# Kernel tuning notes

Hardware: AMD Instinct MI355X
Metric: run time of the kernel (lower is better)

Reference implementation:

```python
import jax, jax.numpy as jnp
import numpy as np

B, C_IN, C_OUT, C_KEY, N = 8, 512, 512, 256, 2048


def setup_inputs() -> dict:
    key = jax.random.key(0)
    k1, k2, k3, k4 = jax.random.split(key, 4)
    x = jax.random.normal(k1, (B, C_IN, N), dtype=jnp.float32)
    # Conv1d(kernel=1, bias=False) weights -> plain linear maps over channel dim
    Wq = jax.random.normal(k2, (C_KEY, C_IN), dtype=jnp.float32) * (1.0 / np.sqrt(C_IN))
    Wk = jax.random.normal(k3, (C_KEY, C_IN), dtype=jnp.float32) * (1.0 / np.sqrt(C_IN))
    Wv = jax.random.normal(k4, (C_OUT, C_IN), dtype=jnp.float32) * (1.0 / np.sqrt(C_IN))
    return {"x": x, "Wq": Wq, "Wk": Wk, "Wv": Wv}


def reference(x, Wq, Wk, Wv):
    # 1x1 conv projections: [B, C, N] -> [B, Ck/Co, N]
    q = jnp.einsum("oc,bcn->bon", Wq, x)
    k = jnp.einsum("oc,bcn->bon", Wk, x)
    v = jnpqv = jnp.einsum("oc,bcn->bon", Wv, x)
    # sim_map[b,i,j] = sum_c k[b,c,i] * q[b,c,j]  (unscaled)
    sim = jnp.einsum("bci,bcj->bij", k, q)  # [B, N, N]
    attn = jax.nn.softmax(sim, axis=-1)
    # out = value @ sim_map, then permute(0,2,1) -> [B, N, C_out]
    out = jnp.einsum("bck,bkm->bmc", jnpqv, attn)
    return out
```

## Files before the change

### kernel.cpp

```cpp
#include <hip/hip_runtime.h>

typedef _Float16 half8 __attribute__((ext_vector_type(8)));
typedef _Float16 half4v __attribute__((ext_vector_type(4)));
typedef _Float16 half2v __attribute__((ext_vector_type(2)));
typedef float f32x4 __attribute__((ext_vector_type(4)));

#define ASYNC_CP16(gp, lp)                                       \
  __builtin_amdgcn_global_load_lds(                              \
      (const __attribute__((address_space(1))) void*)(gp),       \
      (__attribute__((address_space(3))) void*)(lp), 16, 0, 0)

static __device__ __forceinline__ half8 mulw(half8 a, half8 s) {
  half8 o;
#pragma unroll
  for (int j = 0; j < 8; j++) o[j] = a[j] * s[j];
  return o;
}

__global__ __launch_bounds__(256) void conv_w(const float* __restrict__ Wq,
                                              const float* __restrict__ Wk,
                                              const float* __restrict__ Wv,
                                              _Float16* __restrict__ Wb) {
  int idx = blockIdx.x * 256 + threadIdx.x;
  int row = idx >> 9;
  float v;
  if (row < 256)      v = Wq[idx];
  else if (row < 512) v = Wk[idx - 256 * 512];
  else                v = Wv[idx - 512 * 512];
  Wb[idx] = (_Float16)v;
}

__global__ __launch_bounds__(256) void conv_xT(const float* __restrict__ x,
                                               _Float16* __restrict__ xT) {
  __shared__ float T[32][33];
  const int b = blockIdx.z;
  const int n0 = blockIdx.x * 32, c0 = blockIdx.y * 32;
  const int t = threadIdx.x;
  const float* xb = x + (size_t)b * 512 * 2048;
  const int n2 = t & 15, cr = t >> 4;
#pragma unroll
  for (int r = 0; r < 2; r++) {
    int c = cr + r * 16;
    float2 v = *(const float2*)&xb[(size_t)(c0 + c) * 2048 + n0 + n2 * 2];
    T[c][n2 * 2] = v.x;
    T[c][n2 * 2 + 1] = v.y;
  }
  __syncthreads();
  _Float16* xtb = xT + (size_t)b * 2048 * 512;
  const int c2 = t & 15, nr = t >> 4;
#pragma unroll
  for (int r = 0; r < 2; r++) {
    int n = nr + r * 16;
    half2v h;
    h[0] = (_Float16)T[c2 * 2][n];
    h[1] = (_Float16)T[c2 * 2 + 1][n];
    *(half2v*)&xtb[(size_t)(n0 + n) * 512 + c0 + c2 * 2] = h;
  }
}

template <typename OutT, int BUFS, int MODE>
__global__ __launch_bounds__(256) void gemm_nt(
    const _Float16* __restrict__ A, const _Float16* __restrict__ B,
    OutT* __restrict__ C, OutT* __restrict__ C2, int K, int lda, int ldb,
    int ldc, int ldc2, long sA, long sB, long sC, float* __restrict__ pm,
    float* __restrict__ ps) {
  A += (size_t)blockIdx.z * sA;
  B += (size_t)blockIdx.z * sB;
  C += (size_t)blockIdx.z * sC;
  if constexpr (MODE == 1) C2 += (size_t)blockIdx.z * sC;
  const int m_blk = blockIdx.y * 128, n_blk = blockIdx.x * 128;

  __shared__ _Float16 As[BUFS][4096];
  __shared__ _Float16 Bs[BUFS][4096];

  const int t = threadIdx.x;
  const int lane = t & 63, wave = t >> 6;
  const int quad = lane >> 4, l16 = lane & 15;
  const int wm = (wave & 1) * 64, wn = (wave >> 1) * 64;

  const int srow = 16 * wave + (lane >> 2);
  const int schunk = (lane & 3) ^ ((lane >> 3) & 3);
  const _Float16* gA0 = A + (size_t)(m_blk + srow) * lda + schunk * 8;
  const _Float16* gA1 = gA0 + (size_t)64 * lda;
  const _Float16* gB0 = B + (size_t)(n_blk + srow) * ldb + schunk * 8;
  const _Float16* gB1 = gB0 + (size_t)64 * ldb;
  const int lofs = wave * 512 + lane * 8;

  const int rchunk = (quad ^ ((l16 >> 1) & 3)) * 8;

  f32x4 acc[4][4] = {};

#pragma unroll
  for (int pb = 0; pb < BUFS - 1; pb++) {
    if (pb * 32 < K) {
      ASYNC_CP16(gA0 + pb * 32, &As[pb][lofs]);
      ASYNC_CP16(gA1 + pb * 32, &As[pb][lofs + 2048]);
      ASYNC_CP16(gB0 + pb * 32, &Bs[pb][lofs]);
      ASYNC_CP16(gB1 + pb * 32, &Bs[pb][lofs + 2048]);
    }
  }

  int ib = 0;
  for (int k0 = 0; k0 < K; k0 += 32) {
    if constexpr (BUFS == 3) {
      if (k0 + 32 < K)
        asm volatile("s_waitcnt vmcnt(4)\n\ts_barrier" ::: "memory");
      else
        asm volatile("s_waitcnt vmcnt(0)\n\ts_barrier" ::: "memory");
    } else {
      asm volatile("s_waitcnt vmcnt(0)\n\ts_barrier" ::: "memory");
    }
    if (k0 + (BUFS - 1) * 32 < K) {
      int nb = ib + BUFS - 1;
      if (nb >= BUFS) nb -= BUFS;
      const int ko = k0 + (BUFS - 1) * 32;
      ASYNC_CP16(gA0 + ko, &As[nb][lofs]);
      ASYNC_CP16(gA1 + ko, &As[nb][lofs + 2048]);
      ASYNC_CP16(gB0 + ko, &Bs[nb][lofs]);
      ASYNC_CP16(gB1 + ko, &Bs[nb][lofs + 2048]);
    }
    half8 af[4], bf[4];
#pragma unroll
    for (int i = 0; i < 4; i++) {
      af[i] = *(const half8*)&As[ib][(wm + i * 16 + l16) * 32 + rchunk];
      bf[i] = *(const half8*)&Bs[ib][(wn + i * 16 + l16) * 32 + rchunk];
    }
#pragma unroll
    for (int i = 0; i < 4; i++)
#pragma unroll
      for (int j = 0; j < 4; j++)
        acc[i][j] =
            __builtin_amdgcn_mfma_f32_16x16x32_f16(af[i], bf[j], acc[i][j], 0, 0, 0);
    ib++;
    if (ib == BUFS) ib = 0;
  }

  if constexpr (MODE == 2) {
#pragma unroll
    for (int j = 0; j < 4; j++) {
      const int n0 = n_blk + wn + j * 16 + l16;
      float mx = acc[0][j][0];
#pragma unroll
      for (int i = 0; i < 4; i++)
#pragma unroll
        for (int r = 0; r < 4; r++) mx = fmaxf(mx, acc[i][j][r]);
      mx = fmaxf(mx, __shfl_xor(mx, 16, 64));
      mx = fmaxf(mx, __shfl_xor(mx, 32, 64));
      float es = 0.f;
#pragma unroll
      for (int i = 0; i < 4; i++) {
        const int m0 = m_blk + wm + i * 16 + quad * 4;
#pragma unroll
        for (int r = 0; r < 4; r++) {
          _Float16 h = (_Float16)__expf(acc[i][j][r] - mx);
          C[(size_t)(m0 + r) * ldc + n0] = h;
          es += (float)h;
        }
      }
      es += __shfl_xor(es, 16, 64);
      es += __shfl_xor(es, 32, 64);
      if (quad == 0) {
        size_t o =
            ((size_t)blockIdx.z * 32 + blockIdx.y * 2 + (wave & 1)) * 2048 + n0;
        pm[o] = mx;
        ps[o] = es;
      }
    }
  } else {
#pragma unroll
    for (int i = 0; i < 4; i++) {
      const int m0 = m_blk + wm + i * 16 + quad * 4;
#pragma unroll
      for (int j = 0; j < 4; j++) {
        const int n0 = n_blk + wn + j * 16 + l16;
        if constexpr (MODE == 1) {
          if (m_blk < 512) {
            half4v h;
#pragma unroll
            for (int r = 0; r < 4; r++) h[r] = (_Float16)acc[i][j][r];
            *(half4v*)&C[(size_t)n0 * ldc + m0] = h;
          } else {
#pragma unroll
            for (int r = 0; r < 4; r++)
              C2[(size_t)(m0 - 512 + r) * ldc2 + n0] = (OutT)acc[i][j][r];
          }
        } else {
#pragma unroll
          for (int r = 0; r < 4; r++)
            C[(size_t)(m0 + r) * ldc + n0] = (OutT)acc[i][j][r];
        }
      }
    }
  }
}

__global__ __launch_bounds__(256) void colstats2(const float* __restrict__ pm,
                                                 const float* __restrict__ ps,
                                                 _Float16* __restrict__ scl) {
  const int idx = blockIdx.x * 256 + threadIdx.x;
  const int b = idx >> 11, col = idx & 2047;
  const float* pmb = pm + (size_t)b * 32 * 2048 + col;
  const float* psb = ps + (size_t)b * 32 * 2048 + col;
  float pv[32];
  float m = -3.0e38f;
#pragma unroll
  for (int i = 0; i < 32; i++) {
    pv[i] = pmb[(size_t)i * 2048];
    m = fmaxf(m, pv[i]);
  }
  float s = 0.f;
#pragma unroll
  for (int i = 0; i < 32; i++) {
    pv[i] = __expf(pv[i] - m);
    s += psb[(size_t)i * 2048] * pv[i];
  }
  const float inv = 1.0f / s;
  _Float16* so = scl + (size_t)b * 32 * 2048 + col;
#pragma unroll
  for (int i = 0; i < 32; i++) so[(size_t)i * 2048] = (_Float16)(pv[i] * inv);
}

__global__ __launch_bounds__(256) void gemm_av(const _Float16* __restrict__ P,
                                               const _Float16* __restrict__ V,
                                               const _Float16* __restrict__ scl,
                                               float* __restrict__ C,
                                               int cbatch) {
  int lin = blockIdx.x, z, idx;
  if (cbatch == 8) {
    z = lin & 7;
    idx = lin >> 3;
  } else {
    z = lin >> 6;
    idx = lin & 63;
  }
  const int n_blk = (idx & 3) * 128;
  const int m_blk = (idx >> 2) * 128;
  P += (size_t)z * 2048 * 2048;
  V += (size_t)z * 512 * 2048;
  scl += ((size_t)z * 32 + (m_blk >> 6)) * 2048;
  C += (size_t)z * 2048 * 512;

  __shared__ _Float16 As[2][4096];
  __shared__ _Float16 Bs[3][4096];

  const int t = threadIdx.x;
  const int lane = t & 63, wave = t >> 6;
  const int quad = lane >> 4, l16 = lane & 15;
  const int wm = (wave & 1) * 64, wn = (wave >> 1) * 64;

  const int srow = 16 * wave + (lane >> 2);
  const int schunk = (lane & 3) ^ ((lane >> 3) & 3);
  const _Float16* gA0 = P + (size_t)(m_blk + srow) * 2048 + schunk * 8;
  const _Float16* gA1 = gA0 + (size_t)64 * 2048;
  const _Float16* gB0 = V + (size_t)(n_blk + srow) * 2048 + schunk * 8;
  const _Float16* gB1 = gB0 + (size_t)64 * 2048;
  const _Float16* gS0 = scl + schunk * 8;
  const _Float16* gS1 = gS0 + 2048;
  const int lofs = wave * 512 + lane * 8;
  const int rchunk = (quad ^ ((l16 >> 1) & 3)) * 8;

  f32x4 acc[4][4] = {};

  ASYNC_CP16(gB0, &Bs[0][lofs]);
  ASYNC_CP16(gB1, &Bs[0][lofs + 2048]);
  ASYNC_CP16(gB0 + 32, &Bs[1][lofs]);
  ASYNC_CP16(gB1 + 32, &Bs[1][lofs + 2048]);
  {
    half8 a0 = *(const half8*)gA0;
    half8 a1 = *(const half8*)gA1;
    half8 s0 = *(const half8*)gS0;
    half8 s1 = *(const half8*)gS1;
    *(half8*)&As[0][lofs] = mulw(a0, s0);
    *(half8*)&As[0][lofs + 2048] = mulw(a1, s1);
  }
  half8 an0 = *(const half8*)(gA0 + 32);
  half8 an1 = *(const half8*)(gA1 + 32);
  half8 sn0 = *(const half8*)(gS0 + 32);
  half8 sn1 = *(const half8*)(gS1 + 32);
  __syncthreads();

  int ibA = 0, ibB = 0;
  for (int k0 = 0; k0 < 2048; k0 += 32) {
    const bool m1 = (k0 + 32 < 2048), m2 = (k0 + 64 < 2048);
    if (m2) {
      int nb = ibB + 2;
      if (nb >= 3) nb -= 3;
      ASYNC_CP16(gB0 + k0 + 64, &Bs[nb][lofs]);
      ASYNC_CP16(gB1 + k0 + 64, &Bs[nb][lofs + 2048]);
    }
    half8 a20, a21, s20, s21;
    if (m2) {
      a20 = *(const half8*)(gA0 + k0 + 64);
      a21 = *(const half8*)(gA1 + k0 + 64);
      s20 = *(const half8*)(gS0 + k0 + 64);
      s21 = *(const half8*)(gS1 + k0 + 64);
    }
    half8 af[4], bf[4];
#pragma unroll
    for (int i = 0; i < 4; i++) {
      af[i] = *(const half8*)&As[ibA][(wm + i * 16 + l16) * 32 + rchunk];
      bf[i] = *(const half8*)&Bs[ibB][(wn + i * 16 + l16) * 32 + rchunk];
    }
#pragma unroll
    for (int i = 0; i < 4; i++)
#pragma unroll
      for (int j = 0; j < 4; j++)
        acc[i][j] =
            __builtin_amdgcn_mfma_f32_16x16x32_f16(af[i], bf[j], acc[i][j], 0, 0, 0);
    if (m1) {
      *(half8*)&As[ibA ^ 1][lofs] = mulw(an0, sn0);
      *(half8*)&As[ibA ^ 1][lofs + 2048] = mulw(an1, sn1);
      if (m2) {
        an0 = a20;
        an1 = a21;
        sn0 = s20;
        sn1 = s21;
      }
      asm volatile("s_waitcnt vmcnt(6) lgkmcnt(0)\n\ts_barrier" ::: "memory");
    }
    ibA ^= 1;
    ibB++;
    if (ibB == 3) ibB = 0;
  }

#pragma unroll
  for (int i = 0; i < 4; i++) {
    const int m0 = m_blk + wm + i * 16 + quad * 4;
#pragma unroll
    for (int j = 0; j < 4; j++) {
      const int n0 = n_blk + wn + j * 16 + l16;
#pragma unroll
      for (int r = 0; r < 4; r++) C[(size_t)(m0 + r) * 512 + n0] = acc[i][j][r];
    }
  }
}

extern "C" void kernel_launch(void* const* d_in, const int* in_sizes, int n_in,
                              void* d_out, int out_size, void* d_ws,
                              size_t ws_size, hipStream_t stream) {
  const float* x = (const float*)d_in[0];
  const float* Wq = (const float*)d_in[1];
  const float* Wk = (const float*)d_in[2];
  const float* Wv = (const float*)d_in[3];
  float* out = (float*)d_out;

  char* p = (char*)d_ws;
  auto alloc = [&](size_t bytes) -> char* {
    char* r = p;
    p += (bytes + 255) & ~(size_t)255;
    return r;
  };
  const size_t NB = 8, N = 2048, CIN = 512, CO = 512;
  _Float16* Wb = (_Float16*)alloc(1024 * 512 * sizeof(_Float16));
  _Float16* xT = (_Float16*)alloc(NB * N * CIN * sizeof(_Float16));
  _Float16* qkT = (_Float16*)alloc(NB * N * 512 * sizeof(_Float16));
  _Float16* v = (_Float16*)alloc(NB * CO * N * sizeof(_Float16));
  size_t base_used = (size_t)(p - (char*)d_ws);

  const size_t per_b =
      (size_t)N * N * 2 + 2 * 32 * N * 4 + 32 * N * 2 + 8192;
  int cb = 8;
  while (cb > 1 && base_used + (size_t)cb * per_b > ws_size) cb >>= 1;
  _Float16* simH = (_Float16*)alloc((size_t)cb * N * N * 2);
  float* pm = (float*)alloc((size_t)cb * 32 * N * 4);
  float* ps = (float*)alloc((size_t)cb * 32 * N * 4);
  _Float16* scl = (_Float16*)alloc((size_t)cb * 32 * N * 2);

  conv_w<<<dim3(1024 * 512 / 256), 256, 0, stream>>>(Wq, Wk, Wv, Wb);
  conv_xT<<<dim3(64, 16, 8), 256, 0, stream>>>(x, xT);

  gemm_nt<_Float16, 3, 1><<<dim3(16, 8, 8), 256, 0, stream>>>(
      Wb, xT, qkT, v, 512, 512, 512, 512, 2048, 0, (long)(N * CIN),
      (long)(N * 512), nullptr, nullptr);

  for (int b0 = 0; b0 < 8; b0 += cb) {
    const _Float16* qT = qkT + (size_t)b0 * N * 512;
    const _Float16* kT = qkT + (size_t)b0 * N * 512 + 256;
    gemm_nt<_Float16, 2, 2><<<dim3(16, 16, cb), 256, 0, stream>>>(
        qT, kT, simH, nullptr, 256, 512, 512, 2048, 0, (long)(N * 512),
        (long)(N * 512), (long)(N * N), pm, ps);
    colstats2<<<dim3(cb * 8), 256, 0, stream>>>(pm, ps, scl);
    gemm_av<<<dim3(64 * cb), 256, 0, stream>>>(
        simH, v + (size_t)b0 * CO * N, scl, out + (size_t)b0 * N * CO, cb);
  }
}
```

Baseline: 212.4 us.

## Load P operand fragments directly from global into registers, dropping A LDS tile

The P·V GEMM kernel no longer stages the scaled P tile through shared memory. Each wave now loads its own MFMA A-fragments (four rows of 16) straight from global memory into registers, two steps ahead, and applies the per-row scale before the MFMAs. This removes the LDS writes, the LDS reads and part of the barrier traffic for A, and frees shared memory. The cost is duplicate global loads across the two waves that share the same rows, less coalesced fragment-shaped loads, and more registers held in flight.

```diff
diff --git a/kernel.cpp b/kernel.cpp
--- a/kernel.cpp
+++ b/kernel.cpp
@@ -240,7 +240,6 @@
   scl += ((size_t)z * 32 + (m_blk >> 6)) * 2048;
   C += (size_t)z * 2048 * 512;
 
-  __shared__ _Float16 As[2][4096];
   __shared__ _Float16 Bs[3][4096];
 
   const int t = threadIdx.x;
@@ -250,14 +249,13 @@
 
   const int srow = 16 * wave + (lane >> 2);
   const int schunk = (lane & 3) ^ ((lane >> 3) & 3);
-  const _Float16* gA0 = P + (size_t)(m_blk + srow) * 2048 + schunk * 8;
-  const _Float16* gA1 = gA0 + (size_t)64 * 2048;
   const _Float16* gB0 = V + (size_t)(n_blk + srow) * 2048 + schunk * 8;
   const _Float16* gB1 = gB0 + (size_t)64 * 2048;
-  const _Float16* gS0 = scl + schunk * 8;
-  const _Float16* gS1 = gS0 + 2048;
   const int lofs = wave * 512 + lane * 8;
   const int rchunk = (quad ^ ((l16 >> 1) & 3)) * 8;
+
+  const _Float16* gA = P + (size_t)(m_blk + wm + l16) * 2048 + quad * 8;
+  const _Float16* gS = scl + (wm >> 6) * 2048 + quad * 8;
 
   f32x4 acc[4][4] = {};
 
@@ -265,62 +263,60 @@
   ASYNC_CP16(gB1, &Bs[0][lofs + 2048]);
   ASYNC_CP16(gB0 + 32, &Bs[1][lofs]);
   ASYNC_CP16(gB1 + 32, &Bs[1][lofs + 2048]);
-  {
-    half8 a0 = *(const half8*)gA0;
-    half8 a1 = *(const half8*)gA1;
-    half8 s0 = *(const half8*)gS0;
-    half8 s1 = *(const half8*)gS1;
-    *(half8*)&As[0][lofs] = mulw(a0, s0);
-    *(half8*)&As[0][lofs + 2048] = mulw(a1, s1);
-  }
-  half8 an0 = *(const half8*)(gA0 + 32);
-  half8 an1 = *(const half8*)(gA1 + 32);
-  half8 sn0 = *(const half8*)(gS0 + 32);
-  half8 sn1 = *(const half8*)(gS1 + 32);
-  __syncthreads();
-
-  int ibA = 0, ibB = 0;
+  asm volatile("" ::: "memory");
+  half8 ac0 = *(const half8*)(gA);
+  half8 ac1 = *(const half8*)(gA + 16 * 2048);
+  half8 ac2 = *(const half8*)(gA + 32 * 2048);
+  half8 ac3 = *(const half8*)(gA + 48 * 2048);
+  half8 scc = *(const half8*)(gS);
+  half8 an0 = *(const half8*)(gA + 32);
+  half8 an1 = *(const half8*)(gA + 16 * 2048 + 32);
+  half8 an2 = *(const half8*)(gA + 32 * 2048 + 32);
+  half8 an3 = *(const half8*)(gA + 48 * 2048 + 32);
+  half8 scn = *(const half8*)(gS + 32);
+  asm volatile("s_waitcnt vmcnt(0)\n\ts_barrier" ::: "memory");
+
+  int ib = 0;
   for (int k0 = 0; k0 < 2048; k0 += 32) {
-    const bool m1 = (k0 + 32 < 2048), m2 = (k0 + 64 < 2048);
+    const bool m2 = (k0 + 64 < 2048);
+    half8 a20, a21, a22, a23, s2;
     if (m2) {
-      int nb = ibB + 2;
+      int nb = ib + 2;
       if (nb >= 3) nb -= 3;
       ASYNC_CP16(gB0 + k0 + 64, &Bs[nb][lofs]);
       ASYNC_CP16(gB1 + k0 + 64, &Bs[nb][lofs + 2048]);
-    }
-    half8 a20, a21, s20, s21;
-    if (m2) {
-      a20 = *(const half8*)(gA0 + k0 + 64);
-      a21 = *(const half8*)(gA1 + k0 + 64);
-      s20 = *(const half8*)(gS0 + k0 + 64);
-      s21 = *(const half8*)(gS1 + k0 + 64);
-    }
-    half8 af[4], bf[4];
-#pragma unroll
-    for (int i = 0; i < 4; i++) {
-      af[i] = *(const half8*)&As[ibA][(wm + i * 16 + l16) * 32 + rchunk];
-      bf[i] = *(const half8*)&Bs[ibB][(wn + i * 16 + l16) * 32 + rchunk];
-    }
+      asm volatile("" ::: "memory");
+      a20 = *(const half8*)(gA + k0 + 64);
+      a21 = *(const half8*)(gA + 16 * 2048 + k0 + 64);
+      a22 = *(const half8*)(gA + 32 * 2048 + k0 + 64);
+      a23 = *(const half8*)(gA + 48 * 2048 + k0 + 64);
+      s2 = *(const half8*)(gS + k0 + 64);
+    }
+    half8 bf[4];
+#pragma unroll
+    for (int j = 0; j < 4; j++)
+      bf[j] = *(const half8*)&Bs[ib][(wn + j * 16 + l16) * 32 + rchunk];
+    half8 am[4];
+    am[0] = mulw(ac0, scc);
+    am[1] = mulw(ac1, scc);
+    am[2] = mulw(ac2, scc);
+    am[3] = mulw(ac3, scc);
 #pragma unroll
     for (int i = 0; i < 4; i++)
 #pragma unroll
       for (int j = 0; j < 4; j++)
         acc[i][j] =
-            __builtin_amdgcn_mfma_f32_16x16x32_f16(af[i], bf[j], acc[i][j], 0, 0, 0);
-    if (m1) {
-      *(half8*)&As[ibA ^ 1][lofs] = mulw(an0, sn0);
-      *(half8*)&As[ibA ^ 1][lofs + 2048] = mulw(an1, sn1);
-      if (m2) {
-        an0 = a20;
-        an1 = a21;
-        sn0 = s20;
-        sn1 = s21;
-      }
-      asm volatile("s_waitcnt vmcnt(6) lgkmcnt(0)\n\ts_barrier" ::: "memory");
-    }
-    ibA ^= 1;
-    ibB++;
-    if (ibB == 3) ibB = 0;
+            __builtin_amdgcn_mfma_f32_16x16x32_f16(am[i], bf[j], acc[i][j], 0, 0, 0);
+    ac0 = an0; ac1 = an1; ac2 = an2; ac3 = an3; scc = scn;
+    if (m2) { an0 = a20; an1 = a21; an2 = a22; an3 = a23; scn = s2; }
+    if (k0 + 32 < 2048) {
+      if (m2)
+        asm volatile("s_waitcnt vmcnt(12) lgkmcnt(0)\n\ts_barrier" ::: "memory");
+      else
+        asm volatile("s_waitcnt vmcnt(0) lgkmcnt(0)\n\ts_barrier" ::: "memory");
+    }
+    ib++;
+    if (ib == 3) ib = 0;
   }
 
 #pragma unroll
```

Result: slower. 233.5 us (+9.9%).

## Make gemm_av waves independent: per-wave LDS tiles, direct B register loads, no barriers

Applied to the files above, without the earlier changes.

Restructures the P·V GEMM so each wave stages only its own 64-row slice of the scaled P tile in a private LDS double buffer. V fragments are loaded directly from global memory into registers in MFMA layout instead of through shared async copies. This removes all block-wide barriers, and the kernel adds s_setprio around the MFMA block and requests two blocks per CU via launch bounds. In exchange, each wave reloads operands that were previously shared across waves, which raises global/L2 traffic and register pressure, and the B loads are only one step ahead of use.

```diff
diff --git a/kernel.cpp b/kernel.cpp
--- a/kernel.cpp
+++ b/kernel.cpp
@@ -220,11 +220,9 @@
   for (int i = 0; i < 32; i++) so[(size_t)i * 2048] = (_Float16)(pv[i] * inv);
 }
 
-__global__ __launch_bounds__(256) void gemm_av(const _Float16* __restrict__ P,
-                                               const _Float16* __restrict__ V,
-                                               const _Float16* __restrict__ scl,
-                                               float* __restrict__ C,
-                                               int cbatch) {
+__global__ __launch_bounds__(256, 2) void gemm_av(
+    const _Float16* __restrict__ P, const _Float16* __restrict__ V,
+    const _Float16* __restrict__ scl, float* __restrict__ C, int cbatch) {
   int lin = blockIdx.x, z, idx;
   if (cbatch == 8) {
     z = lin & 7;
@@ -237,90 +235,84 @@
   const int m_blk = (idx >> 2) * 128;
   P += (size_t)z * 2048 * 2048;
   V += (size_t)z * 512 * 2048;
-  scl += ((size_t)z * 32 + (m_blk >> 6)) * 2048;
+  scl += (size_t)z * 32 * 2048;
   C += (size_t)z * 2048 * 512;
 
-  __shared__ _Float16 As[2][4096];
-  __shared__ _Float16 Bs[3][4096];
+  __shared__ _Float16 As[4][2][2048];
 
   const int t = threadIdx.x;
   const int lane = t & 63, wave = t >> 6;
   const int quad = lane >> 4, l16 = lane & 15;
   const int wm = (wave & 1) * 64, wn = (wave >> 1) * 64;
 
-  const int srow = 16 * wave + (lane >> 2);
-  const int schunk = (lane & 3) ^ ((lane >> 3) & 3);
-  const _Float16* gA0 = P + (size_t)(m_blk + srow) * 2048 + schunk * 8;
-  const _Float16* gA1 = gA0 + (size_t)64 * 2048;
-  const _Float16* gB0 = V + (size_t)(n_blk + srow) * 2048 + schunk * 8;
-  const _Float16* gB1 = gB0 + (size_t)64 * 2048;
-  const _Float16* gS0 = scl + schunk * 8;
-  const _Float16* gS1 = gS0 + 2048;
-  const int lofs = wave * 512 + lane * 8;
+  const int kc = (lane & 3) ^ ((lane >> 3) & 3);
+  const _Float16* gA = P + (size_t)(m_blk + wm + (lane >> 2)) * 2048 + kc * 8;
+  const _Float16* gS =
+      scl + (size_t)((m_blk + wm) >> 6) * 2048 + kc * 8;
+  const _Float16* gB = V + (size_t)(n_blk + wn + l16) * 2048 + quad * 8;
+
+  const int sofs = lane * 8;
   const int rchunk = (quad ^ ((l16 >> 1) & 3)) * 8;
+  _Float16* myA = &As[wave][0][0];
 
   f32x4 acc[4][4] = {};
 
-  ASYNC_CP16(gB0, &Bs[0][lofs]);
-  ASYNC_CP16(gB1, &Bs[0][lofs + 2048]);
-  ASYNC_CP16(gB0 + 32, &Bs[1][lofs]);
-  ASYNC_CP16(gB1 + 32, &Bs[1][lofs + 2048]);
   {
-    half8 a0 = *(const half8*)gA0;
-    half8 a1 = *(const half8*)gA1;
-    half8 s0 = *(const half8*)gS0;
-    half8 s1 = *(const half8*)gS1;
-    *(half8*)&As[0][lofs] = mulw(a0, s0);
-    *(half8*)&As[0][lofs + 2048] = mulw(a1, s1);
-  }
-  half8 an0 = *(const half8*)(gA0 + 32);
-  half8 an1 = *(const half8*)(gA1 + 32);
-  half8 sn0 = *(const half8*)(gS0 + 32);
-  half8 sn1 = *(const half8*)(gS1 + 32);
-  __syncthreads();
-
-  int ibA = 0, ibB = 0;
+    half8 a0 = *(const half8*)(gA);
+    half8 a1 = *(const half8*)(gA + 16 * 2048);
+    half8 a2 = *(const half8*)(gA + 32 * 2048);
+    half8 a3 = *(const half8*)(gA + 48 * 2048);
+    half8 s0 = *(const half8*)(gS);
+    *(half8*)&myA[sofs] = mulw(a0, s0);
+    *(half8*)&myA[sofs + 512] = mulw(a1, s0);
+    *(half8*)&myA[sofs + 1024] = mulw(a2, s0);
+    *(half8*)&myA[sofs + 1536] = mulw(a3, s0);
+  }
+  half8 b0 = *(const half8*)(gB);
+  half8 b1 = *(const half8*)(gB + 16 * 2048);
+  half8 b2 = *(const half8*)(gB + 32 * 2048);
+  half8 b3 = *(const half8*)(gB + 48 * 2048);
+
+  int p = 0;
   for (int k0 = 0; k0 < 2048; k0 += 32) {
-    const bool m1 = (k0 + 32 < 2048), m2 = (k0 + 64 < 2048);
-    if (m2) {
-      int nb = ibB + 2;
-      if (nb >= 3) nb -= 3;
-      ASYNC_CP16(gB0 + k0 + 64, &Bs[nb][lofs]);
-      ASYNC_CP16(gB1 + k0 + 64, &Bs[nb][lofs + 2048]);
-    }
-    half8 a20, a21, s20, s21;
-    if (m2) {
-      a20 = *(const half8*)(gA0 + k0 + 64);
-      a21 = *(const half8*)(gA1 + k0 + 64);
-      s20 = *(const half8*)(gS0 + k0 + 64);
-      s21 = *(const half8*)(gS1 + k0 + 64);
-    }
-    half8 af[4], bf[4];
+    const bool more = (k0 + 32 < 2048);
+    half8 na0, na1, na2, na3, ns0, nb0, nb1, nb2, nb3;
+    if (more) {
+      na0 = *(const half8*)(gA + k0 + 32);
+      na1 = *(const half8*)(gA + 16 * 2048 + k0 + 32);
+      na2 = *(const half8*)(gA + 32 * 2048 + k0 + 32);
+      na3 = *(const half8*)(gA + 48 * 2048 + k0 + 32);
+      ns0 = *(const half8*)(gS + k0 + 32);
+      nb0 = *(const half8*)(gB + k0 + 32);
+      nb1 = *(const half8*)(gB + 16 * 2048 + k0 + 32);
+      nb2 = *(const half8*)(gB + 32 * 2048 + k0 + 32);
+      nb3 = *(const half8*)(gB + 48 * 2048 + k0 + 32);
+    }
+    half8 af[4];
+#pragma unroll
+    for (int i = 0; i < 4; i++)
+      af[i] = *(const half8*)&myA[p * 2048 + i * 512 + l16 * 32 + rchunk];
+    __builtin_amdgcn_s_setprio(1);
 #pragma unroll
     for (int i = 0; i < 4; i++) {
-      af[i] = *(const half8*)&As[ibA][(wm + i * 16 + l16) * 32 + rchunk];
-      bf[i] = *(const half8*)&Bs[ibB][(wn + i * 16 + l16) * 32 + rchunk];
-    }
-#pragma unroll
-    for (int i = 0; i < 4; i++)
-#pragma unroll
-      for (int j = 0; j < 4; j++)
-        acc[i][j] =
-            __builtin_amdgcn_mfma_f32_16x16x32_f16(af[i], bf[j], acc[i][j], 0, 0, 0);
-    if (m1) {
-      *(half8*)&As[ibA ^ 1][lofs] = mulw(an0, sn0);
-      *(half8*)&As[ibA ^ 1][lofs + 2048] = mulw(an1, sn1);
-      if (m2) {
-        an0 = a20;
-        an1 = a21;
-        sn0 = s20;
-        sn1 = s21;
-      }
-      asm volatile("s_waitcnt vmcnt(6) lgkmcnt(0)\n\ts_barrier" ::: "memory");
-    }
-    ibA ^= 1;
-    ibB++;
-    if (ibB == 3) ibB = 0;
+      acc[i][0] = __builtin_amdgcn_mfma_f32_16x16x32_f16(af[i], b0, acc[i][0], 0, 0, 0);
+      acc[i][1] = __builtin_amdgcn_mfma_f32_16x16x32_f16(af[i], b1, acc[i][1], 0, 0, 0);
+      acc[i][2] = __builtin_amdgcn_mfma_f32_16x16x32_f16(af[i], b2, acc[i][2], 0, 0, 0);
+      acc[i][3] = __builtin_amdgcn_mfma_f32_16x16x32_f16(af[i], b3, acc[i][3], 0, 0, 0);
+    }
+    __builtin_amdgcn_s_setprio(0);
+    if (more) {
+      _Float16* dst = &myA[(p ^ 1) * 2048];
+      *(half8*)&dst[sofs] = mulw(na0, ns0);
+      *(half8*)&dst[sofs + 512] = mulw(na1, ns0);
+      *(half8*)&dst[sofs + 1024] = mulw(na2, ns0);
+      *(half8*)&dst[sofs + 1536] = mulw(na3, ns0);
+      b0 = nb0;
+      b1 = nb1;
+      b2 = nb2;
+      b3 = nb3;
+    }
+    p ^= 1;
   }
 
 #pragma unroll
```

Measured after the change: 238.6 us. +12.3%, slower.

## Widen gemm_av tile to 128x256 with 512-thread blocks to halve P rereads

Applied to the files above, without the earlier changes.

The attention-times-value GEMM now uses 512-thread blocks, each computing a 128x256 output tile instead of 128x128. Each block covers twice as many output columns, so the large fp16 probability matrix and its scales are read half as many times from global memory. Load indexing and the wait counters are adjusted for one A row per thread. In exchange the grid is halved to one block per CU, and LDS per block grows to 64KB, which lowers occupancy and latency hiding.

```diff
diff --git a/kernel.cpp b/kernel.cpp
--- a/kernel.cpp
+++ b/kernel.cpp
@@ -70,8 +70,8 @@
   if constexpr (MODE == 1) C2 += (size_t)blockIdx.z * sC;
   const int m_blk = blockIdx.y * 128, n_blk = blockIdx.x * 128;
 
-  __shared__ _Float16 As[BUFS][4096];
-  __shared__ _Float16 Bs[BUFS][4096];
+  __shared__ __align__(16) _Float16 As[BUFS][4096];
+  __shared__ __align__(16) _Float16 Bs[BUFS][4096];
 
   const int t = threadIdx.x;
   const int lane = t & 63, wave = t >> 6;
@@ -220,7 +220,7 @@
   for (int i = 0; i < 32; i++) so[(size_t)i * 2048] = (_Float16)(pv[i] * inv);
 }
 
-__global__ __launch_bounds__(256) void gemm_av(const _Float16* __restrict__ P,
+__global__ __launch_bounds__(512) void gemm_av(const _Float16* __restrict__ P,
                                                const _Float16* __restrict__ V,
                                                const _Float16* __restrict__ scl,
                                                float* __restrict__ C,
@@ -230,54 +230,48 @@
     z = lin & 7;
     idx = lin >> 3;
   } else {
-    z = lin >> 6;
-    idx = lin & 63;
-  }
-  const int n_blk = (idx & 3) * 128;
-  const int m_blk = (idx >> 2) * 128;
+    z = lin >> 5;
+    idx = lin & 31;
+  }
+  const int n_blk = (idx & 1) * 256;
+  const int m_blk = (idx >> 1) * 128;
   P += (size_t)z * 2048 * 2048;
   V += (size_t)z * 512 * 2048;
-  scl += ((size_t)z * 32 + (m_blk >> 6)) * 2048;
+  scl += (size_t)z * 32 * 2048;
   C += (size_t)z * 2048 * 512;
 
-  __shared__ _Float16 As[2][4096];
-  __shared__ _Float16 Bs[3][4096];
+  __shared__ __align__(16) _Float16 As[2][4096];
+  __shared__ __align__(16) _Float16 Bs[3][8192];
 
   const int t = threadIdx.x;
   const int lane = t & 63, wave = t >> 6;
   const int quad = lane >> 4, l16 = lane & 15;
   const int wm = (wave & 1) * 64, wn = (wave >> 1) * 64;
 
-  const int srow = 16 * wave + (lane >> 2);
-  const int schunk = (lane & 3) ^ ((lane >> 3) & 3);
-  const _Float16* gA0 = P + (size_t)(m_blk + srow) * 2048 + schunk * 8;
-  const _Float16* gA1 = gA0 + (size_t)64 * 2048;
+  const int srow = t >> 2;
+  const int schunk = (t & 3) ^ ((t >> 3) & 3);
+  const _Float16* gA = P + (size_t)(m_blk + srow) * 2048 + schunk * 8;
+  const _Float16* gS =
+      scl + (size_t)((m_blk + srow) >> 6) * 2048 + schunk * 8;
   const _Float16* gB0 = V + (size_t)(n_blk + srow) * 2048 + schunk * 8;
-  const _Float16* gB1 = gB0 + (size_t)64 * 2048;
-  const _Float16* gS0 = scl + schunk * 8;
-  const _Float16* gS1 = gS0 + 2048;
-  const int lofs = wave * 512 + lane * 8;
+  const _Float16* gB1 = gB0 + (size_t)128 * 2048;
+  const int lofs = t * 8;
   const int rchunk = (quad ^ ((l16 >> 1) & 3)) * 8;
 
   f32x4 acc[4][4] = {};
 
   ASYNC_CP16(gB0, &Bs[0][lofs]);
-  ASYNC_CP16(gB1, &Bs[0][lofs + 2048]);
+  ASYNC_CP16(gB1, &Bs[0][lofs + 4096]);
   ASYNC_CP16(gB0 + 32, &Bs[1][lofs]);
-  ASYNC_CP16(gB1 + 32, &Bs[1][lofs + 2048]);
+  ASYNC_CP16(gB1 + 32, &Bs[1][lofs + 4096]);
   {
-    half8 a0 = *(const half8*)gA0;
-    half8 a1 = *(const half8*)gA1;
-    half8 s0 = *(const half8*)gS0;
-    half8 s1 = *(const half8*)gS1;
+    half8 a0 = *(const half8*)gA;
+    half8 s0 = *(const half8*)gS;
     *(half8*)&As[0][lofs] = mulw(a0, s0);
-    *(half8*)&As[0][lofs + 2048] = mulw(a1, s1);
-  }
-  half8 an0 = *(const half8*)(gA0 + 32);
-  half8 an1 = *(const half8*)(gA1 + 32);
-  half8 sn0 = *(const half8*)(gS0 + 32);
-  half8 sn1 = *(const half8*)(gS1 + 32);
-  __syncthreads();
+  }
+  half8 an0 = *(const half8*)(gA + 32);
+  half8 sn0 = *(const half8*)(gS + 32);
+  asm volatile("s_waitcnt vmcnt(0)\n\ts_barrier" ::: "memory");
 
   int ibA = 0, ibB = 0;
   for (int k0 = 0; k0 < 2048; k0 += 32) {
@@ -286,14 +280,12 @@
       int nb = ibB + 2;
       if (nb >= 3) nb -= 3;
       ASYNC_CP16(gB0 + k0 + 64, &Bs[nb][lofs]);
-      ASYNC_CP16(gB1 + k0 + 64, &Bs[nb][lofs + 2048]);
-    }
-    half8 a20, a21, s20, s21;
+      ASYNC_CP16(gB1 + k0 + 64, &Bs[nb][lofs + 4096]);
+    }
+    half8 a2, s2;
     if (m2) {
-      a20 = *(const half8*)(gA0 + k0 + 64);
-      a21 = *(const half8*)(gA1 + k0 + 64);
-      s20 = *(const half8*)(gS0 + k0 + 64);
-      s21 = *(const half8*)(gS1 + k0 + 64);
+      a2 = *(const half8*)(gA + k0 + 64);
+      s2 = *(const half8*)(gS + k0 + 64);
     }
     half8 af[4], bf[4];
 #pragma unroll
@@ -309,14 +301,11 @@
             __builtin_amdgcn_mfma_f32_16x16x32_f16(af[i], bf[j], acc[i][j], 0, 0, 0);
     if (m1) {
       *(half8*)&As[ibA ^ 1][lofs] = mulw(an0, sn0);
-      *(half8*)&As[ibA ^ 1][lofs + 2048] = mulw(an1, sn1);
       if (m2) {
-        an0 = a20;
-        an1 = a21;
-        sn0 = s20;
-        sn1 = s21;
+        an0 = a2;
+        sn0 = s2;
       }
-      asm volatile("s_waitcnt vmcnt(6) lgkmcnt(0)\n\ts_barrier" ::: "memory");
+      asm volatile("s_waitcnt vmcnt(4) lgkmcnt(0)\n\ts_barrier" ::: "memory");
     }
     ibA ^= 1;
     ibB++;
@@ -380,7 +369,7 @@
         qT, kT, simH, nullptr, 256, 512, 512, 2048, 0, (long)(N * 512),
         (long)(N * 512), (long)(N * N), pm, ps);
     colstats2<<<dim3(cb * 8), 256, 0, stream>>>(pm, ps, scl);
-    gemm_av<<<dim3(64 * cb), 256, 0, stream>>>(
+    gemm_av<<<dim3(32 * cb), 512, 0, stream>>>(
         simH, v + (size_t)b0 * CO * N, scl, out + (size_t)b0 * N * CO, cb);
   }
 }
```

Measured after the change: 215.8 us. No clear change (+1.6%).
